# Kernel tuning notes

Hardware: AMD Instinct MI355X
Metric: run time of the kernel (lower is better)

Reference implementation:

```python
import jax, jax.numpy as jnp
import numpy as np

T, N = 128, 2048
D_LIN, D_AC, D_IM = 300, 74, 35
H_LIN, H_AC, H_IM = 88, 48, 88
TOT_H = H_LIN + H_AC + H_IM          # 224
ATT_IN = 2 * TOT_H                   # 448 (window_dim=2)
MEM = 128
GAMMA_IN = ATT_IN + MEM              # 576
FINAL = TOT_H + MEM                  # 352
OUT_DIM = 1


def _lin(x, w, b):
    # torch nn.Linear: y = x @ W^T + b, W: [out, in]
    return x @ w.T + b


def _lstm_cell(x, h, c, w_ih, w_hh, b_ih, b_hh):
    # torch nn.LSTMCell gate order: i, f, g, o
    gates = x @ w_ih.T + b_ih + h @ w_hh.T + b_hh
    i, f, g, o = jnp.split(gates, 4, axis=-1)
    c2 = jax.nn.sigmoid(f) * c + jax.nn.sigmoid(i) * jnp.tanh(g)
    h2 = jax.nn.sigmoid(o) * jnp.tanh(c2)
    return h2, c2


def _forward(x_lin, x_ac, x_im, p):
    (W_ih_lin, W_hh_lin, b_ih_lin, b_hh_lin,
     W_ih_ac, W_hh_ac, b_ih_ac, b_hh_ac,
     W_ih_im, W_hh_im, b_ih_im, b_hh_im,
     att1_w1, att1_b1, att1_w2, att1_b2,
     att2_w1, att2_b1, att2_w2, att2_b2,
     g1_w1, g1_b1, g1_w2, g1_b2,
     g2_w1, g2_b1, g2_w2, g2_b2,
     out_w1, out_b1, out_w2, out_b2) = p
    n = x_lin.shape[1]
    z = lambda d: jnp.zeros((n, d), dtype=x_lin.dtype)
    init = (z(H_LIN), z(H_LIN), z(H_AC), z(H_AC), z(H_IM), z(H_IM), z(MEM))

    def step(carry, xs):
        h_l, c_l, h_a, c_a, h_i, c_i, mem = carry
        xl, xa, xi = xs
        nh_l, nc_l = _lstm_cell(xl, h_l, c_l, W_ih_lin, W_hh_lin, b_ih_lin, b_hh_lin)
        nh_a, nc_a = _lstm_cell(xa, h_a, c_a, W_ih_ac, W_hh_ac, b_ih_ac, b_hh_ac)
        nh_i, nc_i = _lstm_cell(xi, h_i, c_i, W_ih_im, W_hh_im, b_ih_im, b_hh_im)
        prev_cs = jnp.concatenate([c_l, c_a, c_i], axis=1)
        new_cs = jnp.concatenate([nc_l, nc_a, nc_i], axis=1)
        c_star = jnp.concatenate([prev_cs, new_cs], axis=1)   # [n, 448]
        attn = jax.nn.softmax(
            _lin(jax.nn.relu(_lin(c_star, att1_w1, att1_b1)), att1_w2, att1_b2), axis=1)
        attended = attn * c_star
        c_hat = jnp.tanh(
            _lin(jax.nn.relu(_lin(attended, att2_w1, att2_b1)), att2_w2, att2_b2))
        both = jnp.concatenate([attended, mem], axis=1)       # [n, 576]
        gamma1 = jax.nn.sigmoid(_lin(jax.nn.relu(_lin(both, g1_w1, g1_b1)), g1_w2, g1_b2))
        gamma2 = jax.nn.sigmoid(_lin(jax.nn.relu(_lin(both, g2_w1, g2_b1)), g2_w2, g2_b2))
        new_mem = gamma1 * mem + gamma2 * c_hat
        return ((nh_l, nc_l, nh_a, nc_a, nh_i, nc_i, new_mem),
                (nh_l, nh_a, nh_i, new_mem))

    _, (hs_l, hs_a, hs_i, mems) = jax.lax.scan(step, init, (x_lin, x_ac, x_im))
    feats = jnp.concatenate([hs_l, hs_a, hs_i, mems], axis=-1)  # [T, n, 352]
    out = _lin(jax.nn.relu(_lin(feats, out_w1, out_b1)), out_w2, out_b2)  # [T, n, 1]
    return jnp.transpose(out, (1, 0, 2))  # [n, T, 1] (torch cats over dim=1)


def setup_inputs() -> dict:
    key = jax.random.key(0)
    ks = iter(jax.random.split(key, 64))

    def rn(shape, s=0.05):
        return (jax.random.normal(next(ks), shape) * s).astype(jnp.float32)

    inp = {
        'x_linguistic': rn((T, N, D_LIN), 1.0),
        'x_acoustic': rn((T, N, D_AC), 1.0),
        'x_image': rn((T, N, D_IM), 1.0),
    }
    for name, din, h in [('lin', D_LIN, H_LIN), ('ac', D_AC, H_AC), ('im', D_IM, H_IM)]:
        inp[f'W_ih_{name}'] = rn((4 * h, din))
        inp[f'W_hh_{name}'] = rn((4 * h, h))
        inp[f'b_ih_{name}'] = rn((4 * h,))
        inp[f'b_hh_{name}'] = rn((4 * h,))
    for nm, hdim, din, dout in [('att1', 128, ATT_IN, ATT_IN),
                                ('att2', 256, ATT_IN, MEM),
                                ('g1', 64, GAMMA_IN, MEM),
                                ('g2', 64, GAMMA_IN, MEM),
                                ('out', 64, FINAL, OUT_DIM)]:
        inp[f'{nm}_w1'] = rn((hdim, din))
        inp[f'{nm}_b1'] = rn((hdim,))
        inp[f'{nm}_w2'] = rn((dout, hdim))
        inp[f'{nm}_b2'] = rn((dout,))
    return inp


def reference(x_linguistic, x_acoustic, x_image,
              W_ih_lin, W_hh_lin, b_ih_lin, b_hh_lin,
              W_ih_ac, W_hh_ac, b_ih_ac, b_hh_ac,
              W_ih_im, W_hh_im, b_ih_im, b_hh_im,
              att1_w1, att1_b1, att1_w2, att1_b2,
              att2_w1, att2_b1, att2_w2, att2_b2,
              g1_w1, g1_b1, g1_w2, g1_b2,
              g2_w1, g2_b1, g2_w2, g2_b2,
              out_w1, out_b1, out_w2, out_b2):
    p = (W_ih_lin, W_hh_lin, b_ih_lin, b_hh_lin,
         W_ih_ac, W_hh_ac, b_ih_ac, b_hh_ac,
         W_ih_im, W_hh_im, b_ih_im, b_hh_im,
         att1_w1, att1_b1, att1_w2, att1_b2,
         att2_w1, att2_b1, att2_w2, att2_b2,
         g1_w1, g1_b1, g1_w2, g1_b2,
         g2_w1, g2_b1, g2_w2, g2_b2,
         out_w1, out_b1, out_w2, out_b2)
    return _forward(x_linguistic, x_acoustic, x_image, p)
```

## Files before the change

kernel.cpp:

```cpp
#include <hip/hip_runtime.h>


#define T_STEPS 128

typedef __attribute__((ext_vector_type(8))) short bf16x8;
typedef __attribute__((ext_vector_type(4))) float f32x4;
typedef __attribute__((ext_vector_type(2))) unsigned long long ull2;

#define MFMA_B16(a,b,c) __builtin_amdgcn_mfma_f32_16x16x32_bf16((a),(b),(c),0,0,0)

__device__ __forceinline__ unsigned short f2b(float v) {
  union { float f; unsigned u; } x; x.f = v;
  unsigned r = x.u + 0x7fffu + ((x.u >> 16) & 1u);
  return (unsigned short)(r >> 16);
}
__device__ __forceinline__ float b2f(unsigned short u) {
  union { unsigned u; float f; } x; x.u = ((unsigned)u) << 16; return x.f;
}
__device__ __forceinline__ float sigm(float x){ return 1.0f/(1.0f + __expf(-x)); }
__device__ __forceinline__ float tanh_(float x){ return 1.0f - 2.0f/(1.0f + __expf(2.0f*x)); }

#define OFF_XL     0
#define OFF_XA     10496
#define OFF_XI     13824
#define OFF_CSTAR  16128
#define OFF_ATT    30720
#define OFF_HID    45312
#define OFF_G1H    53760
#define OFF_G2H    56064
#define OFF_FEATS  58368
#define OFF_BIAS   69888
#define OFF_XP     79368
#define LDS_BYTES  110344

#define BG_LIN 0
#define BG_AC  384
#define BG_IM  576
#define B_A1H  960
#define B_LOG  1088
#define B_A2H  1536
#define B_CHAT 1792
#define B_G1H  1920
#define B_G2H  1984
#define B_GM1  2048
#define B_GM2  2176
#define B_OUTH 2304
#define B_OUT2 2368
#define N_BIAS 2369

#define N_TILES 1718
#define PACK_BYTES ((size_t)N_TILES * 1024)
#define XP_ELEMS ((size_t)262144 * 960)
#define XP_BYTES (XP_ELEMS * 2)

#define LA(off,st,row,kk)  (*(const bf16x8*)(lds + (off) + ((((row)*(st)) + (kk)) << 1)))
#define LB(tile)           (*(const bf16x8*)(packc + (((size_t)(tile)) << 10) + (lane << 4)))
#define STB(off,st,row,col,v) (*(unsigned short*)(lds + (off) + ((((row)*(st)) + (col)) << 1)) = f2b(v))
#define LDB(off,st,row,col)   b2f(*(const unsigned short*)(lds + (off) + ((((row)*(st)) + (col)) << 1)))

struct PP { const float* p[35]; };

__device__ __forceinline__ void vmw(int n) {
  switch (n) {
    case 0: asm volatile("s_waitcnt vmcnt(0)"); break;
    case 1: asm volatile("s_waitcnt vmcnt(1)"); break;
    case 2: asm volatile("s_waitcnt vmcnt(2)"); break;
    case 3: asm volatile("s_waitcnt vmcnt(3)"); break;
    case 4: asm volatile("s_waitcnt vmcnt(4)"); break;
    case 5: asm volatile("s_waitcnt vmcnt(5)"); break;
    case 6: asm volatile("s_waitcnt vmcnt(6)"); break;
    default: asm volatile("s_waitcnt vmcnt(7)"); break;
  }
  __builtin_amdgcn_sched_barrier(0);
}

#define ISSUE_B(dst, tile)                                                   \
  { unsigned off_ = (((unsigned)(tile)) << 10) + ((unsigned)lane << 4);      \
    asm volatile("global_load_dwordx4 %0, %1, %2"                            \
                 : "=v"(dst) : "v"(off_), "s"(packc)); }

template<int NTT, class FT, class FB>
__device__ __forceinline__ void reg_loop(const char* packc, int lane,
                                         FT&& tile_of, FB&& body)
{
  constexpr int D = (NTT < 8) ? NTT : 8;
  bf16x8 b[8];
  #pragma unroll
  for (int i = 0; i < D; ++i) ISSUE_B(b[i], tile_of(i));
  #pragma unroll
  for (int i = 0; i < NTT; ++i) {
    vmw((NTT-1-i) < 7 ? (NTT-1-i) : 7);
    body(i, b[i & 7]);
    __builtin_amdgcn_sched_barrier(0);
    if (i + 8 < NTT) ISSUE_B(b[i & 7], tile_of(i + 8));
  }
}

__device__ __forceinline__ float gate_src(const float* Wih, const float* Whh,
                                          int H, int din, int nksx, int col, int k)
{
  int blk = col >> 6, gate = (col >> 4) & 3, u = col & 15;
  int unit = blk*16 + u;
  if (unit >= H) return 0.f;
  int row = gate*H + unit;
  int xk = nksx*32;
  if (k < xk) return (k < din) ? Wih[row*din + k] : 0.f;
  int kk = k - xk;
  return (kk < H) ? Whh[row*H + kk] : 0.f;
}
__device__ __forceinline__ float gate_h(const float* Whh, int H, int col, int k)
{
  int blk = col >> 6, gate = (col >> 4) & 3, u = col & 15;
  int unit = blk*16 + u;
  if (unit >= H || k >= H) return 0.f;
  return Whh[(gate*H + unit)*H + k];
}
__device__ __forceinline__ float gate_x(const float* Wih, int H, int din, int col, int k)
{
  int blk = col >> 6, gate = (col >> 4) & 3, u = col & 15;
  int unit = blk*16 + u;
  if (unit >= H || k >= din) return 0.f;
  return Wih[(gate*H + unit)*din + k];
}
__device__ __forceinline__ float plain_src(const float* W, int nout, int kdim, int col, int k)
{
  return (col < nout && k < kdim) ? W[col*kdim + k] : 0.f;
}

__global__ __launch_bounds__(256) void pack_kernel(PP P, unsigned short* __restrict__ pack,
                                                   float* __restrict__ bias)
{
  int tid = blockIdx.x*blockDim.x + threadIdx.x;
  int wv = tid >> 6, lane = tid & 63;
  int nw = (gridDim.x*blockDim.x) >> 6;
  int c = lane & 15, kg = lane >> 4;

  for (int tile = wv; tile < N_TILES; tile += nw) {
    unsigned short* dst = pack + ((size_t)tile << 9) + lane*8;
    #pragma unroll
    for (int i = 0; i < 8; ++i) {
      int r = tile; int nt, ks; float v; int kk;
      if (r < 312)       { nt=r/13; ks=r-nt*13; kk=ks*32+kg*8+i; v = gate_src(P.p[3], P.p[4], 88,300,10, nt*16+c, kk); }
      else if (r < 372)  { r-=312; nt=r/5;  ks=r-nt*5;  kk=ks*32+kg*8+i; v = gate_src(P.p[7], P.p[8], 48, 74, 3, nt*16+c, kk); }
      else if (r < 492)  { r-=372; nt=r/5;  ks=r-nt*5;  kk=ks*32+kg*8+i; v = gate_src(P.p[11],P.p[12],88, 35, 2, nt*16+c, kk); }
      else if (r < 604)  { r-=492; nt=r/14; ks=r-nt*14; kk=ks*32+kg*8+i; v = plain_src(P.p[15],128,448, nt*16+c, kk); }
      else if (r < 716)  { r-=604; nt=r/4;  ks=r-nt*4;  kk=ks*32+kg*8+i; v = plain_src(P.p[17],448,128, nt*16+c, kk); }
      else if (r < 940)  { r-=716; nt=r/14; ks=r-nt*14; kk=ks*32+kg*8+i; v = plain_src(P.p[19],256,448, nt*16+c, kk); }
      else if (r < 1004) { r-=940; nt=r/8;  ks=r-nt*8;  kk=ks*32+kg*8+i; v = plain_src(P.p[21],128,256, nt*16+c, kk); }
      else if (r < 1076) { r-=1004; nt=r/18; ks=r-nt*18; kk=ks*32+kg*8+i; v = plain_src(P.p[23], 64,576, nt*16+c, kk); }
      else if (r < 1148) { r-=1076; nt=r/18; ks=r-nt*18; kk=ks*32+kg*8+i; v = plain_src(P.p[27], 64,576, nt*16+c, kk); }
      else if (r < 1164) { r-=1148; nt=r/2;  ks=r-nt*2;  kk=ks*32+kg*8+i; v = plain_src(P.p[25],128, 64, nt*16+c, kk); }
      else if (r < 1180) { r-=1164; nt=r/2;  ks=r-nt*2;  kk=ks*32+kg*8+i; v = plain_src(P.p[29],128, 64, nt*16+c, kk); }
      else if (r < 1224) { r-=1180; nt=r/11; ks=r-nt*11; kk=ks*32+kg*8+i; v = plain_src(P.p[31], 64,352, nt*16+c, kk); }
      else if (r < 1226) { r-=1224; ks=r;    kk=ks*32+kg*8+i; v = plain_src(P.p[33],  1, 64, c, kk); }
      else if (r < 1298) { r-=1226; nt=r/3;  ks=r-nt*3;  kk=ks*32+kg*8+i; v = gate_h(P.p[4], 88, nt*16+c, kk); }
      else if (r < 1322) { r-=1298; nt=r/2;  ks=r-nt*2;  kk=ks*32+kg*8+i; v = gate_h(P.p[8], 48, nt*16+c, kk); }
      else if (r < 1394) { r-=1322; nt=r/3;  ks=r-nt*3;  kk=ks*32+kg*8+i; v = gate_h(P.p[12],88, nt*16+c, kk); }
      else if (r < 1634) { r-=1394; nt=r/10; ks=r-nt*10; kk=ks*32+kg*8+i; v = gate_x(P.p[3], 88,300, nt*16+c, kk); }
      else if (r < 1670) { r-=1634; nt=r/3;  ks=r-nt*3;  kk=ks*32+kg*8+i; v = gate_x(P.p[7], 48, 74, nt*16+c, kk); }
      else               { r-=1670; nt=r/2;  ks=r-nt*2;  kk=ks*32+kg*8+i; v = gate_x(P.p[11],88, 35, nt*16+c, kk); }
      dst[i] = f2b(v);
    }
  }

  int NT = gridDim.x*blockDim.x;
  for (int b = tid; b < N_BIAS; b += NT) {
    float v; int r = b;
    if (r < 384)       { int blk=r>>6, g=(r>>4)&3, u=r&15, un=blk*16+u; v = (un<88) ? P.p[5][g*88+un] + P.p[6][g*88+un]  : 0.f; }
    else if (r < 576)  { r-=384; int blk=r>>6, g=(r>>4)&3, u=r&15, un=blk*16+u; v = (un<48) ? P.p[9][g*48+un] + P.p[10][g*48+un] : 0.f; }
    else if (r < 960)  { r-=576; int blk=r>>6, g=(r>>4)&3, u=r&15, un=blk*16+u; v = (un<88) ? P.p[13][g*88+un]+ P.p[14][g*88+un] : 0.f; }
    else if (r < 1088) v = P.p[16][r-960];
    else if (r < 1536) v = P.p[18][r-1088];
    else if (r < 1792) v = P.p[20][r-1536];
    else if (r < 1920) v = P.p[22][r-1792];
    else if (r < 1984) v = P.p[24][r-1920];
    else if (r < 2048) v = P.p[28][r-1984];
    else if (r < 2176) v = P.p[26][r-2048];
    else if (r < 2304) v = P.p[30][r-2176];
    else if (r < 2368) v = P.p[32][r-2304];
    else               v = P.p[34][0];
    bias[b] = v;
  }
}

__global__ __launch_bounds__(1024) void xproj_kernel(
    const float* __restrict__ xlin, const float* __restrict__ xac,
    const float* __restrict__ xim, const unsigned short* __restrict__ pack,
    unsigned short* __restrict__ xp)
{
  __shared__ alignas(16) char slds[81920];
  const char* packc = (const char*)pack;
  const int tid = threadIdx.x, lane = tid & 63, w = tid >> 6;
  const int rA = lane & 15, gA = lane >> 4;
  const int mt = w & 7, half = w >> 3;
  const size_t m0 = (size_t)blockIdx.x * 128;
  const int mr = mt * 16;

  for (int p = tid; p < 9600; p += 1024) {
    int row = p/75, d = p - row*75;
    float4 v = *(const float4*)(xlin + (m0+row)*300 + d*4);
    unsigned long long u = (unsigned long long)f2b(v.x)
      | ((unsigned long long)f2b(v.y) << 16)
      | ((unsigned long long)f2b(v.z) << 32)
      | ((unsigned long long)f2b(v.w) << 48);
    *(unsigned long long*)(slds + (((size_t)row*320 + d*4) << 1)) = u;
  }
  for (int p = tid; p < 1280; p += 1024) {
    int row = p/10, cc = 300 + 2*(p - row*10);
    *(unsigned*)(slds + (((size_t)row*320 + cc) << 1)) = 0;
  }
  __syncthreads();
  for (int blk = half*3; blk < half*3 + 3; ++blk) {
    #pragma unroll
    for (int q = 0; q < 4; ++q) {
      f32x4 acc = {0.f,0.f,0.f,0.f};
      int nt = blk*4 + q;
      bf16x8 a = *(const bf16x8*)(slds + ((((mr+rA)*320) + gA*8) << 1));
      reg_loop<10>(packc, lane,
        [&](int i){ return 1394 + nt*10 + i; },
        [&](int i, bf16x8 bv){
          acc = MFMA_B16(a, bv, acc);
          if (i + 1 < 10) a = *(const bf16x8*)(slds + ((((mr+rA)*320) + (i+1)*32 + gA*8) << 1));
        });
      #pragma unroll
      for (int j = 0; j < 4; ++j)
        xp[(m0 + mr + gA*4 + j)*960 + blk*64 + q*16 + rA] = f2b(acc[j]);
    }
  }
  __syncthreads();

  for (int p = tid; p < 4736; p += 1024) {
    int row = p/37, d = p - row*37;
    float2 v = *(const float2*)(xac + (m0+row)*74 + d*2);
    unsigned uu = (unsigned)f2b(v.x) | ((unsigned)f2b(v.y) << 16);
    *(unsigned*)(slds + (((size_t)row*96 + d*2) << 1)) = uu;
  }
  for (int p = tid; p < 1408; p += 1024) {
    int row = p/11, cc = 74 + 2*(p - row*11);
    *(unsigned*)(slds + (((size_t)row*96 + cc) << 1)) = 0;
  }
  __syncthreads();
  if (half == 0) {
    for (int blk = 0; blk < 3; ++blk) {
      #pragma unroll
      for (int q = 0; q < 4; ++q) {
        f32x4 acc = {0.f,0.f,0.f,0.f};
        int nt = blk*4 + q;
        bf16x8 a = *(const bf16x8*)(slds + ((((mr+rA)*96) + gA*8) << 1));
        reg_loop<3>(packc, lane,
          [&](int i){ return 1634 + nt*3 + i; },
          [&](int i, bf16x8 bv){
            acc = MFMA_B16(a, bv, acc);
            if (i + 1 < 3) a = *(const bf16x8*)(slds + ((((mr+rA)*96) + (i+1)*32 + gA*8) << 1));
          });
        #pragma unroll
        for (int j = 0; j < 4; ++j)
          xp[(m0 + mr + gA*4 + j)*960 + 384 + blk*64 + q*16 + rA] = f2b(acc[j]);
      }
    }
  }
  __syncthreads();

  for (int p = tid; p < 4480; p += 1024) {
    int row = p/35, d = p - row*35;
    *(unsigned short*)(slds + (((size_t)row*64 + d) << 1)) = f2b(xim[(m0+row)*35 + d]);
  }
  for (int p = tid; p < 3712; p += 1024) {
    int row = p/29, cc = 35 + (p - row*29);
    *(unsigned short*)(slds + (((size_t)row*64 + cc) << 1)) = 0;
  }
  __syncthreads();
  if (half == 1) {
    for (int blk = 0; blk < 6; ++blk) {
      #pragma unroll
      for (int q = 0; q < 4; ++q) {
        f32x4 acc = {0.f,0.f,0.f,0.f};
        int nt = blk*4 + q;
        bf16x8 a = *(const bf16x8*)(slds + ((((mr+rA)*64) + gA*8) << 1));
        reg_loop<2>(packc, lane,
          [&](int i){ return 1670 + nt*2 + i; },
          [&](int i, bf16x8 bv){
            acc = MFMA_B16(a, bv, acc);
            if (i + 1 < 2) a = *(const bf16x8*)(slds + ((((mr+rA)*64) + 32 + gA*8) << 1));
          });
        #pragma unroll
        for (int j = 0; j < 4; ++j)
          xp[(m0 + mr + gA*4 + j)*960 + 576 + blk*64 + q*16 + rA] = f2b(acc[j]);
      }
    }
  }
}

template<int NKS>
__device__ __forceinline__ void gate_reg_h(f32x4 acc[4], const char* lds, const char* packc,
    int lane, int rA, int gA, int hsec, int tb)
{
  bf16x8 a;
  reg_loop<NKS*4>(packc, lane,
    [&](int i){ return tb + (i & 3)*NKS + (i >> 2); },
    [&](int i, bf16x8 bv){
      int q = i & 3, s = i >> 2;
      if (q == 0) a = LA(OFF_FEATS, 360, rA, hsec + s*32 + gA*8);
      acc[q] = MFMA_B16(a, bv, acc[q]);
    });
}

__device__ __forceinline__ void stage_xp(char* lds, const unsigned short* __restrict__ xp,
                                         int t, int n0, int tid0, int nthr)
{
  const size_t base = ((size_t)t*2048 + n0)*960;
  for (int q = tid0; q < 1920; q += nthr) {
    int row = q/120, ch = q - row*120;
    ull2 v = __builtin_nontemporal_load((const ull2*)(xp + base + (size_t)row*960 + ch*8));
    *(ull2*)(lds + OFF_XP + (((size_t)row*968 + ch*8) << 1)) = v;
  }
}

__global__ __launch_bounds__(1024) void fused_kernel(
    const unsigned short* __restrict__ pack, const float* __restrict__ biasg,
    const unsigned short* __restrict__ xp, float* __restrict__ out)
{
  __shared__ alignas(16) char lds[LDS_BYTES];
  const char* packc = (const char*)pack;
  const int tid  = threadIdx.x;
  const int lane = tid & 63;
  const int w    = tid >> 6;
  const int rA   = lane & 15;
  const int gA   = lane >> 4;
  const int n0   = blockIdx.x * 16;
  float* biasLds = (float*)(lds + OFF_BIAS);

  for (int i = tid; i < (OFF_BIAS >> 2); i += 1024) ((int*)lds)[i] = 0;
  __syncthreads();
  for (int i = tid; i < N_BIAS; i += 1024) biasLds[i] = biasg[i];
  stage_xp(lds, xp, 0, n0, tid, 1024);
  __syncthreads();

  float cst[4]  = {};
  float mreg[4] = {};

  for (int t = 0; t < T_STEPS; ++t) {
    f32x4 gacc[4];
    if (w == 15) {
      if (t > 0) {
        float bv = biasLds[B_OUT2];
        f32x4 oa0 = {bv,bv,bv,bv};
        bf16x8 as[2], bs[2];
        #pragma unroll
        for (int s = 0; s < 2; ++s) { bs[s] = LB(1224 + s); as[s] = LA(OFF_HID,72, rA, s*32+gA*8); }
        #pragma unroll
        for (int s = 0; s < 2; ++s) oa0 = MFMA_B16(as[s], bs[s], oa0);
        if (rA == 0) {
          #pragma unroll
          for (int j = 0; j < 4; ++j)
            __builtin_nontemporal_store(oa0[j], &out[(size_t)(n0 + gA*4 + j)*T_STEPS + (t-1)]);
        }
      }
    } else {
      int blk, tb, nks, hsec, bb, cb;
      if (w < 6)      { blk=w;   tb=1226+w*12;      nks=3; hsec=0;   bb=BG_LIN; cb=0   + w*64; }
      else if (w < 9) { blk=w-6; tb=1298+(w-6)*8;   nks=2; hsec=88;  bb=BG_AC;  cb=384 + (w-6)*64; }
      else            { blk=w-9; tb=1322+(w-9)*12;  nks=3; hsec=136; bb=BG_IM;  cb=576 + (w-9)*64; }
      #pragma unroll
      for (int q = 0; q < 4; ++q) {
        float bv = biasLds[bb + blk*64 + q*16 + rA];
        #pragma unroll
        for (int j = 0; j < 4; ++j) {
          int row = gA*4 + j;
          float xv = b2f(*(const unsigned short*)(lds + OFF_XP + (((size_t)row*968 + cb + q*16 + rA) << 1)));
          gacc[q][j] = bv + xv;
        }
      }
      if (nks == 3) gate_reg_h<3>(gacc, lds, packc, lane, rA, gA, hsec, tb);
      else          gate_reg_h<2>(gacc, lds, packc, lane, rA, gA, hsec, tb);
    }
    __syncthreads();

    if (w < 15) {
      int blk, hsec, H;
      if (w < 6)      { blk=w;   hsec=0;   H=88; }
      else if (w < 9) { blk=w-6; hsec=88;  H=48; }
      else            { blk=w-9; hsec=136; H=88; }
      int unit = blk*16 + rA;
      if (unit < H) {
        #pragma unroll
        for (int j = 0; j < 4; ++j) {
          float iv = sigm (gacc[0][j]);
          float fv = sigm (gacc[1][j]);
          float gv = tanh_(gacc[2][j]);
          float ov = sigm (gacc[3][j]);
          float cp = cst[j];
          float cn = fv*cp + iv*gv;
          float hn = ov*tanh_(cn);
          cst[j] = cn;
          int row = gA*4 + j;
          STB(OFF_CSTAR,456, row, hsec + unit,        cp);
          STB(OFF_CSTAR,456, row, 224 + hsec + unit,  cn);
          STB(OFF_FEATS,360, row, hsec + unit,        hn);
        }
      }
    }
    __syncthreads();

    if (w < 8) {
      int n = w;
      float bv = biasLds[B_A1H + n*16 + rA];
      f32x4 a0v = {bv,bv,bv,bv};
      bf16x8 a = LA(OFF_CSTAR,456, rA, gA*8);
      reg_loop<14>(packc, lane,
        [&](int i){ return 492 + n*14 + i; },
        [&](int i, bf16x8 bv8){
          a0v = MFMA_B16(a, bv8, a0v);
          if (i + 1 < 14) a = LA(OFF_CSTAR,456, rA, (i+1)*32+gA*8);
        });
      #pragma unroll
      for (int j = 0; j < 4; ++j)
        STB(OFF_HID,136, gA*4 + j, n*16 + rA, fmaxf(a0v[j], 0.f));
    }
    __syncthreads();

    {
      float bv1 = biasLds[B_LOG + w*16 + rA];
      if (w < 12) {
        float bv2 = biasLds[B_LOG + (w+16)*16 + rA];
        f32x4 l0 = {bv1,bv1,bv1,bv1}, l1 = {bv2,bv2,bv2,bv2};
        bf16x8 a = LA(OFF_HID,136, rA, gA*8);
        reg_loop<8>(packc, lane,
          [&](int i){ int tau = (i < 4) ? w : (w + 16); return 604 + tau*4 + (i & 3); },
          [&](int i, bf16x8 bv8){
            if (i < 4) l0 = MFMA_B16(a, bv8, l0); else l1 = MFMA_B16(a, bv8, l1);
            if (i + 1 < 8) a = LA(OFF_HID,136, rA, ((i+1)&3)*32+gA*8);
          });
        #pragma unroll
        for (int j = 0; j < 4; ++j) {
          STB(OFF_ATT,456, gA*4 + j, w*16 + rA,      l0[j]);
          STB(OFF_ATT,456, gA*4 + j, (w+16)*16 + rA, l1[j]);
        }
      } else {
        f32x4 l0 = {bv1,bv1,bv1,bv1};
        bf16x8 a = LA(OFF_HID,136, rA, gA*8);
        reg_loop<4>(packc, lane,
          [&](int i){ return 604 + w*4 + i; },
          [&](int i, bf16x8 bv8){
            l0 = MFMA_B16(a, bv8, l0);
            if (i + 1 < 4) a = LA(OFF_HID,136, rA, (i+1)*32+gA*8);
          });
        #pragma unroll
        for (int j = 0; j < 4; ++j)
          STB(OFF_ATT,456, gA*4 + j, w*16 + rA, l0[j]);
      }
    }
    __syncthreads();

    if (w < 8) {
      int row = w*2 + (lane >> 5);
      int cb  = lane & 31;
      float v[14];
      float mx = -3.0e38f;
      #pragma unroll
      for (int q = 0; q < 14; ++q) { v[q] = LDB(OFF_ATT,456,row, cb + 32*q); mx = fmaxf(mx, v[q]); }
      #pragma unroll
      for (int mk = 1; mk < 32; mk <<= 1) mx = fmaxf(mx, __shfl_xor(mx, mk));
      float sm = 0.f;
      #pragma unroll
      for (int q = 0; q < 14; ++q) { v[q] = __expf(v[q] - mx); sm += v[q]; }
      #pragma unroll
      for (int mk = 1; mk < 32; mk <<= 1) sm += __shfl_xor(sm, mk);
      float inv = 1.0f / sm;
      #pragma unroll
      for (int q = 0; q < 14; ++q) {
        int c = cb + 32*q;
        float cs = LDB(OFF_CSTAR,456,row,c);
        STB(OFF_ATT,456,row,c, v[q]*inv*cs);
      }
    } else if (t < T_STEPS-1) {
      stage_xp(lds, xp, t+1, n0, tid - 512, 512);
    }
    __syncthreads();

    if (w >= 8) {
      int nb = (w - 8)*2;
      float b0 = biasLds[B_A2H + nb*16 + rA];
      float b1 = biasLds[B_A2H + (nb+1)*16 + rA];
      f32x4 A0 = {b0,b0,b0,b0}, A1 = {b1,b1,b1,b1};
      bf16x8 a = LA(OFF_ATT,456, rA, gA*8);
      reg_loop<28>(packc, lane,
        [&](int i){ int rr = (i >= 14) ? 1 : 0; int s = i - (rr ? 14 : 0); return 716 + (nb+rr)*14 + s; },
        [&](int i, bf16x8 bv8){
          if (i < 14) A0 = MFMA_B16(a, bv8, A0); else A1 = MFMA_B16(a, bv8, A1);
          if (i + 1 < 28) {
            int ns = (i + 1 < 14) ? (i + 1) : (i + 1 - 14);
            a = LA(OFF_ATT,456, rA, ns*32+gA*8);
          }
        });
      #pragma unroll
      for (int j = 0; j < 4; ++j) {
        STB(OFF_HID,264, gA*4 + j, nb*16 + rA,     fmaxf(A0[j], 0.f));
        STB(OFF_HID,264, gA*4 + j, (nb+1)*16 + rA, fmaxf(A1[j], 0.f));
      }
    } else {
      int which = w >> 2;
      int n = w & 3;
      int tbq = which ? 1076 : 1004;
      int bb  = which ? B_G2H : B_G1H;
      int oo  = which ? OFF_G2H : OFF_G1H;
      float bv = biasLds[bb + n*16 + rA];
      f32x4 A0 = {bv,bv,bv,bv};
      bf16x8 a = LA(OFF_ATT,456, rA, gA*8);
      reg_loop<18>(packc, lane,
        [&](int i){ return tbq + n*18 + i; },
        [&](int i, bf16x8 bv8){
          A0 = MFMA_B16(a, bv8, A0);
          if (i + 1 < 18) {
            a = (i + 1 < 14) ? LA(OFF_ATT,456, rA, (i+1)*32+gA*8)
                             : LA(OFF_FEATS,360, rA, 224 + (i+1-14)*32 + gA*8);
          }
        });
      #pragma unroll
      for (int j = 0; j < 4; ++j)
        STB(oo,72, gA*4 + j, n*16 + rA, fmaxf(A0[j], 0.f));
    }
    __syncthreads();

    if (w < 8) {
      int n = w;
      float bc = biasLds[B_CHAT + n*16 + rA];
      float b1 = biasLds[B_GM1  + n*16 + rA];
      float b2 = biasLds[B_GM2  + n*16 + rA];
      f32x4 cc0={bc,bc,bc,bc};
      f32x4 g10={b1,b1,b1,b1};
      f32x4 g20={b2,b2,b2,b2};
      bf16x8 a = LA(OFF_HID,264, rA, gA*8);
      reg_loop<12>(packc, lane,
        [&](int i){
          if (i < 8)  return 940 + n*8 + i;
          if (i < 10) return 1148 + n*2 + (i - 8);
          return 1164 + n*2 + (i - 10);
        },
        [&](int i, bf16x8 bv8){
          if (i < 8)       cc0 = MFMA_B16(a, bv8, cc0);
          else if (i < 10) g10 = MFMA_B16(a, bv8, g10);
          else             g20 = MFMA_B16(a, bv8, g20);
          if (i + 1 < 8)        a = LA(OFF_HID,264, rA, (i+1)*32+gA*8);
          else if (i + 1 == 8)  a = LA(OFF_G1H,72, rA, gA*8);
          else if (i + 1 == 9)  a = LA(OFF_G1H,72, rA, 32+gA*8);
          else if (i + 1 == 10) a = LA(OFF_G2H,72, rA, gA*8);
          else if (i + 1 == 11) a = LA(OFF_G2H,72, rA, 32+gA*8);
        });
      #pragma unroll
      for (int j = 0; j < 4; ++j) {
        float ch = tanh_(cc0[j]), ga = sigm(g10[j]), gb = sigm(g20[j]);
        float mn = ga*mreg[j] + gb*ch;
        mreg[j] = mn;
        STB(OFF_FEATS,360, gA*4 + j, 224 + n*16 + rA, mn);
      }
    }
    __syncthreads();

    if (w < 4) {
      int n = w;
      float bv = biasLds[B_OUTH + n*16 + rA];
      f32x4 a0v = {bv,bv,bv,bv};
      bf16x8 a = LA(OFF_FEATS,360, rA, gA*8);
      reg_loop<11>(packc, lane,
        [&](int i){ return 1180 + n*11 + i; },
        [&](int i, bf16x8 bv8){
          a0v = MFMA_B16(a, bv8, a0v);
          if (i + 1 < 11) a = LA(OFF_FEATS,360, rA, (i+1)*32+gA*8);
        });
      #pragma unroll
      for (int j = 0; j < 4; ++j)
        STB(OFF_HID,72, gA*4 + j, n*16 + rA, fmaxf(a0v[j], 0.f));
    }
    __syncthreads();
  }

  if (w == 15) {
    float bv = biasLds[B_OUT2];
    f32x4 oa0 = {bv,bv,bv,bv};
    bf16x8 as[2], bs[2];
    #pragma unroll
    for (int s = 0; s < 2; ++s) { bs[s] = LB(1224 + s); as[s] = LA(OFF_HID,72, rA, s*32+gA*8); }
    #pragma unroll
    for (int s = 0; s < 2; ++s) oa0 = MFMA_B16(as[s], bs[s], oa0);
    if (rA == 0) {
      #pragma unroll
      for (int j = 0; j < 4; ++j)
        __builtin_nontemporal_store(oa0[j], &out[(size_t)(n0 + gA*4 + j)*T_STEPS + 127]);
    }
  }
}

extern "C" void kernel_launch(void* const* d_in, const int* in_sizes, int n_in,
                              void* d_out, int out_size, void* d_ws, size_t ws_size,
                              hipStream_t stream) {
  (void)in_sizes; (void)n_in; (void)out_size; (void)ws_size;
  PP P;
  for (int i = 0; i < 35; ++i) P.p[i] = (const float*)d_in[i];
  unsigned short* pack = (unsigned short*)d_ws;
  float* bias = (float*)((char*)d_ws + PACK_BYTES);
  unsigned short* xp = (unsigned short*)((char*)d_ws + PACK_BYTES + 16384);

  hipLaunchKernelGGL(pack_kernel, dim3(320), dim3(256), 0, stream, P, pack, bias);
  hipLaunchKernelGGL(xproj_kernel, dim3(2048), dim3(1024), 0, stream,
                     P.p[0], P.p[1], P.p[2], pack, xp);
  hipLaunchKernelGGL(fused_kernel, dim3(128), dim3(1024), 0, stream,
                     pack, bias, xp, (float*)d_out);
}
```

Baseline: 4.045 ms.

## Keep LSTM recurrent weights in registers and cache attention weights in LDS

The recurrent h-to-gate weight tiles (up to 12 per wave) and the output-layer tiles are loaded into registers once before the time loop, instead of being fetched from global memory on every step. The first 6 of 14 K-tiles of the attention-1 weights for each wave are staged into a new 48 KB LDS region and read from there, while the remaining 8 still stream from global. This targets repeated global/L2 weight traffic inside the sequential 128-step loop. In exchange it raises VGPR pressure at 1024 threads per block and enlarges LDS to about 159 KB.

```diff
diff --git a/kernel.cpp b/kernel.cpp
--- a/kernel.cpp
+++ b/kernel.cpp
@@ -31,7 +31,8 @@
 #define OFF_FEATS  58368
 #define OFF_BIAS   69888
 #define OFF_XP     79368
-#define LDS_BYTES  110344
+#define OFF_WC     110344
+#define LDS_BYTES  159496
 
 #define BG_LIN 0
 #define BG_AC  384
@@ -291,20 +292,6 @@
   }
 }
 
-template<int NKS>
-__device__ __forceinline__ void gate_reg_h(f32x4 acc[4], const char* lds, const char* packc,
-    int lane, int rA, int gA, int hsec, int tb)
-{
-  bf16x8 a;
-  reg_loop<NKS*4>(packc, lane,
-    [&](int i){ return tb + (i & 3)*NKS + (i >> 2); },
-    [&](int i, bf16x8 bv){
-      int q = i & 3, s = i >> 2;
-      if (q == 0) a = LA(OFF_FEATS, 360, rA, hsec + s*32 + gA*8);
-      acc[q] = MFMA_B16(a, bv, acc[q]);
-    });
-}
-
 __device__ __forceinline__ void stage_xp(char* lds, const unsigned short* __restrict__ xp,
                                          int t, int n0, int tid0, int nthr)
 {
@@ -334,7 +321,28 @@
   __syncthreads();
   for (int i = tid; i < N_BIAS; i += 1024) biasLds[i] = biasg[i];
   stage_xp(lds, xp, 0, n0, tid, 1024);
+  for (int idx = tid; idx < 48*64; idx += 1024) {
+    int slot = idx >> 6, l = idx & 63;
+    int nn = slot / 6, ii = slot - nn*6;
+    int tile = 492 + nn*14 + ii;
+    bf16x8 v = *(const bf16x8*)(packc + ((size_t)tile << 10) + (l << 4));
+    *(bf16x8*)(lds + OFF_WC + ((size_t)slot << 10) + (l << 4)) = v;
+  }
   __syncthreads();
+
+  int blkP, tbP, nksP, hsecP, bbP, cbP, HP;
+  if (w < 6)       { blkP=w;   tbP=1226+w*12;     nksP=3; hsecP=0;   bbP=BG_LIN; cbP=0   + w*64;      HP=88; }
+  else if (w < 9)  { blkP=w-6; tbP=1298+(w-6)*8;  nksP=2; hsecP=88;  bbP=BG_AC;  cbP=384 + (w-6)*64;  HP=48; }
+  else if (w < 15) { blkP=w-9; tbP=1322+(w-9)*12; nksP=3; hsecP=136; bbP=BG_IM;  cbP=576 + (w-9)*64;  HP=88; }
+  else             { blkP=0;   tbP=1226;          nksP=3; hsecP=0;   bbP=BG_LIN; cbP=0;               HP=88; }
+
+  bf16x8 gw[12];
+  {
+    int ntile = nksP*4;
+    #pragma unroll
+    for (int i = 0; i < 12; ++i) gw[i] = LB(tbP + (i < ntile ? i : 0));
+  }
+  bf16x8 ow0 = LB(1224), ow1 = LB(1225);
 
   float cst[4]  = {};
   float mreg[4] = {};
@@ -345,11 +353,8 @@
       if (t > 0) {
         float bv = biasLds[B_OUT2];
         f32x4 oa0 = {bv,bv,bv,bv};
-        bf16x8 as[2], bs[2];
-        #pragma unroll
-        for (int s = 0; s < 2; ++s) { bs[s] = LB(1224 + s); as[s] = LA(OFF_HID,72, rA, s*32+gA*8); }
-        #pragma unroll
-        for (int s = 0; s < 2; ++s) oa0 = MFMA_B16(as[s], bs[s], oa0);
+        oa0 = MFMA_B16(LA(OFF_HID,72, rA, gA*8),      ow0, oa0);
+        oa0 = MFMA_B16(LA(OFF_HID,72, rA, 32 + gA*8), ow1, oa0);
         if (rA == 0) {
           #pragma unroll
           for (int j = 0; j < 4; ++j)
@@ -357,32 +362,37 @@
         }
       }
     } else {
-      int blk, tb, nks, hsec, bb, cb;
-      if (w < 6)      { blk=w;   tb=1226+w*12;      nks=3; hsec=0;   bb=BG_LIN; cb=0   + w*64; }
-      else if (w < 9) { blk=w-6; tb=1298+(w-6)*8;   nks=2; hsec=88;  bb=BG_AC;  cb=384 + (w-6)*64; }
-      else            { blk=w-9; tb=1322+(w-9)*12;  nks=3; hsec=136; bb=BG_IM;  cb=576 + (w-9)*64; }
       #pragma unroll
       for (int q = 0; q < 4; ++q) {
-        float bv = biasLds[bb + blk*64 + q*16 + rA];
+        float bv = biasLds[bbP + blkP*64 + q*16 + rA];
         #pragma unroll
         for (int j = 0; j < 4; ++j) {
           int row = gA*4 + j;
-          float xv = b2f(*(const unsigned short*)(lds + OFF_XP + (((size_t)row*968 + cb + q*16 + rA) << 1)));
+          float xv = b2f(*(const unsigned short*)(lds + OFF_XP + (((size_t)row*968 + cbP + q*16 + rA) << 1)));
           gacc[q][j] = bv + xv;
         }
       }
-      if (nks == 3) gate_reg_h<3>(gacc, lds, packc, lane, rA, gA, hsec, tb);
-      else          gate_reg_h<2>(gacc, lds, packc, lane, rA, gA, hsec, tb);
+      if (nksP == 3) {
+        #pragma unroll
+        for (int s = 0; s < 3; ++s) {
+          bf16x8 a = LA(OFF_FEATS,360, rA, hsecP + s*32 + gA*8);
+          #pragma unroll
+          for (int q = 0; q < 4; ++q) gacc[q] = MFMA_B16(a, gw[q*3+s], gacc[q]);
+        }
+      } else {
+        #pragma unroll
+        for (int s = 0; s < 2; ++s) {
+          bf16x8 a = LA(OFF_FEATS,360, rA, hsecP + s*32 + gA*8);
+          #pragma unroll
+          for (int q = 0; q < 4; ++q) gacc[q] = MFMA_B16(a, gw[q*2+s], gacc[q]);
+        }
+      }
     }
     __syncthreads();
 
     if (w < 15) {
-      int blk, hsec, H;
-      if (w < 6)      { blk=w;   hsec=0;   H=88; }
-      else if (w < 9) { blk=w-6; hsec=88;  H=48; }
-      else            { blk=w-9; hsec=136; H=88; }
-      int unit = blk*16 + rA;
-      if (unit < H) {
+      int unit = blkP*16 + rA;
+      if (unit < HP) {
         #pragma unroll
         for (int j = 0; j < 4; ++j) {
           float iv = sigm (gacc[0][j]);
@@ -394,9 +404,9 @@
           float hn = ov*tanh_(cn);
           cst[j] = cn;
           int row = gA*4 + j;
-          STB(OFF_CSTAR,456, row, hsec + unit,        cp);
-          STB(OFF_CSTAR,456, row, 224 + hsec + unit,  cn);
-          STB(OFF_FEATS,360, row, hsec + unit,        hn);
+          STB(OFF_CSTAR,456, row, hsecP + unit,        cp);
+          STB(OFF_CSTAR,456, row, 224 + hsecP + unit,  cn);
+          STB(OFF_FEATS,360, row, hsecP + unit,        hn);
         }
       }
     }
@@ -406,12 +416,17 @@
       int n = w;
       float bv = biasLds[B_A1H + n*16 + rA];
       f32x4 a0v = {bv,bv,bv,bv};
-      bf16x8 a = LA(OFF_CSTAR,456, rA, gA*8);
-      reg_loop<14>(packc, lane,
-        [&](int i){ return 492 + n*14 + i; },
+      #pragma unroll
+      for (int i = 0; i < 6; ++i) {
+        bf16x8 bw = *(const bf16x8*)(lds + OFF_WC + ((size_t)(n*6 + i) << 10) + (lane << 4));
+        bf16x8 a = LA(OFF_CSTAR,456, rA, i*32+gA*8);
+        a0v = MFMA_B16(a, bw, a0v);
+      }
+      reg_loop<8>(packc, lane,
+        [&](int i){ return 492 + n*14 + 6 + i; },
         [&](int i, bf16x8 bv8){
+          bf16x8 a = LA(OFF_CSTAR,456, rA, (6+i)*32+gA*8);
           a0v = MFMA_B16(a, bv8, a0v);
-          if (i + 1 < 14) a = LA(OFF_CSTAR,456, rA, (i+1)*32+gA*8);
         });
       #pragma unroll
       for (int j = 0; j < 4; ++j)
@@ -578,11 +593,8 @@
   if (w == 15) {
     float bv = biasLds[B_OUT2];
     f32x4 oa0 = {bv,bv,bv,bv};
-    bf16x8 as[2], bs[2];
-    #pragma unroll
-    for (int s = 0; s < 2; ++s) { bs[s] = LB(1224 + s); as[s] = LA(OFF_HID,72, rA, s*32+gA*8); }
-    #pragma unroll
-    for (int s = 0; s < 2; ++s) oa0 = MFMA_B16(as[s], bs[s], oa0);
+    oa0 = MFMA_B16(LA(OFF_HID,72, rA, gA*8),      ow0, oa0);
+    oa0 = MFMA_B16(LA(OFF_HID,72, rA, 32 + gA*8), ow1, oa0);
     if (rA == 0) {
       #pragma unroll
       for (int j = 0; j < 4; ++j)
```

New measurement: 5.308 ms. 31.2% more time.
